# Kernel optimization log

Measured on AMD Instinct MI355X. Metric: run time of the kernel, lower is better.

## Reference

```python
import jax, jax.numpy as jnp
import numpy as np

N, D, M = 100000, 128, 2048


def setup_inputs() -> dict:
    key = jax.random.key(0)
    k1, k2, k3, k4 = jax.random.split(key, 4)
    X = jax.random.normal(k1, (N, D), dtype=jnp.float32)
    Y = jax.random.normal(k2, (N, 1), dtype=jnp.float32)
    centers = jax.random.normal(k3, (M, D), dtype=jnp.float32)
    # alpha is a buffer produced by an inner Falkon solve; use small random values
    alpha = jax.random.normal(k4, (M, 1), dtype=jnp.float32) * 0.01
    sigma = jnp.asarray(1.0, dtype=jnp.float32)     # Gaussian kernel lengthscale (nn.Parameter)
    penalty = jnp.asarray(5.0, dtype=jnp.float32)   # lambda = exp(-penalty)
    return {"X": X, "Y": Y, "centers": centers, "alpha": alpha,
            "sigma": sigma, "penalty": penalty}


def _rbf_mmv(A, B, v, sigma):
    # Gaussian (RBF) kernel mat-vec: exp(-||a-b||^2 / (2 sigma^2)) @ v
    # A:[n,d], B:[m,d], v:[m,1] -> [n,1]
    a2 = jnp.sum(A * A, axis=-1, keepdims=True)          # [n,1]
    b2 = jnp.sum(B * B, axis=-1, keepdims=True).T        # [1,m]
    sq = a2 + b2 - 2.0 * (A @ B.T)                       # [n,m] squared distances
    Kmat = jnp.exp(-sq / (2.0 * sigma * sigma))
    return Kmat @ v


def reference(X, Y, centers, alpha, sigma, penalty):
    # loss = mean((K_NM @ alpha - Y)^2) + exp(-penalty) * alpha^T K_MM alpha
    preds = _rbf_mmv(X, centers, alpha, sigma)                     # [N,1]
    loss = jnp.mean((preds - Y) ** 2)
    pen = jnp.exp(-penalty)
    reg = pen * (alpha.T @ _rbf_mmv(centers, centers, alpha, sigma))  # [1,1]
    total = loss + reg[0, 0]
    return total, preds
```

## Files before the change

### kernel.cpp

```cpp
#include <hip/hip_runtime.h>
#include <stdint.h>

typedef short short8 __attribute__((ext_vector_type(8)));
typedef float f32x4 __attribute__((ext_vector_type(4)));

#define TILE 128

__device__ __forceinline__ unsigned short f32_to_bf16(float f) {
    uint32_t u = __builtin_bit_cast(uint32_t, f);
    u += 0x7FFFu + ((u >> 16) & 1u);
    return (unsigned short)(u >> 16);
}
__device__ __forceinline__ float bf16_to_f32(unsigned short h) {
    return __builtin_bit_cast(float, (uint32_t)h << 16);
}

__global__ void prep_kernel(const float* __restrict__ C,
                            const float* __restrict__ alpha,
                            const float* __restrict__ sigma,
                            unsigned short* __restrict__ Bp,
                            float2* __restrict__ cw,
                            float* __restrict__ acc)
{
    const int t = threadIdx.x;
    const int g = blockIdx.x;
    const int r = t >> 4;
    const int c16 = t & 15;
    const int R = g * 16 + r;

    if (g == 0 && t == 0) {
        acc[0] = 0.f; acc[1] = 0.f;
        ((unsigned int*)acc)[2] = 0u;
    }

    const float4* src = (const float4*)(C + (size_t)R * 128 + c16 * 8);
    float4 va = src[0], vb = src[1];
    unsigned short h[8];
    h[0] = f32_to_bf16(va.x); h[1] = f32_to_bf16(va.y);
    h[2] = f32_to_bf16(va.z); h[3] = f32_to_bf16(va.w);
    h[4] = f32_to_bf16(vb.x); h[5] = f32_to_bf16(vb.y);
    h[6] = f32_to_bf16(vb.z); h[7] = f32_to_bf16(vb.w);
    float ss = 0.f;
    #pragma unroll
    for (int k = 0; k < 8; ++k) {
        float f = bf16_to_f32(h[k]);
        ss = fmaf(f, f, ss);
    }
    uint4 pk;
    pk.x = (uint32_t)h[0] | ((uint32_t)h[1] << 16);
    pk.y = (uint32_t)h[2] | ((uint32_t)h[3] << 16);
    pk.z = (uint32_t)h[4] | ((uint32_t)h[5] << 16);
    pk.w = (uint32_t)h[6] | ((uint32_t)h[7] << 16);
    *reinterpret_cast<uint4*>(Bp + (size_t)g * 2048 + c16 * 128 + r * 8) = pk;

    ss += __shfl_xor(ss, 1);
    ss += __shfl_xor(ss, 2);
    ss += __shfl_xor(ss, 4);
    ss += __shfl_xor(ss, 8);
    if (c16 == 0) {
        float sig = sigma[0];
        float q = 0.7213475204444817f / (sig * sig);
        cw[R] = make_float2(ss * q, alpha[R]);
    }
}

__global__ __launch_bounds__(512, 4)
void fused_kernel(const float* __restrict__ X, int N,
                  const float* __restrict__ Yv,
                  const unsigned short* __restrict__ Bp,
                  const float2* __restrict__ cw,
                  const float* __restrict__ alpha,
                  const float* __restrict__ sigma,
                  const float* __restrict__ penalty,
                  int nA, int nMt, int nBlk,
                  float* __restrict__ preds_out,
                  float* __restrict__ out0,
                  float* __restrict__ acc)
{
    __shared__ __align__(16) unsigned short ldsA[16384];
    __shared__ float a2p[TILE][4];
    __shared__ float predbuf[TILE][4];

    const int t    = threadIdx.x;
    const int lane = t & 63;
    const int wid  = t >> 6;
    const int h    = wid & 1;
    const int wq   = wid >> 1;
    const int l15  = lane & 15;
    const int quad = lane >> 4;

    const float sig = sigma[0];
    const float q  = 0.7213475204444817f / (sig * sig);
    const float q2 = 2.0f * q;

    const bool regmode = (int)blockIdx.x >= nA;
    int rowbase;
    float rowterm[4][4];
    short8 a[16];

    if (!regmode) {
        rowbase = blockIdx.x * TILE;
        const int r_  = t >> 2;
        const int qtr = t & 3;
        const int grow = rowbase + r_;
        unsigned short* dstbase = ldsA + (r_ >> 4) * 2048 + (r_ & 15) * 8;
        float ss = 0.f;
        if (grow < N) {
            const float4* src = (const float4*)(X + (size_t)grow * 128 + qtr * 32);
            #pragma unroll
            for (int c = 0; c < 4; ++c) {
                float4 va = src[2 * c], vb = src[2 * c + 1];
                unsigned short h0 = f32_to_bf16(va.x), h1 = f32_to_bf16(va.y);
                unsigned short h2 = f32_to_bf16(va.z), h3 = f32_to_bf16(va.w);
                unsigned short h4 = f32_to_bf16(vb.x), h5 = f32_to_bf16(vb.y);
                unsigned short h6 = f32_to_bf16(vb.z), h7 = f32_to_bf16(vb.w);
                float f0 = bf16_to_f32(h0), f1 = bf16_to_f32(h1);
                float f2 = bf16_to_f32(h2), f3 = bf16_to_f32(h3);
                float f4 = bf16_to_f32(h4), f5 = bf16_to_f32(h5);
                float f6 = bf16_to_f32(h6), f7 = bf16_to_f32(h7);
                ss = fmaf(f0, f0, ss); ss = fmaf(f1, f1, ss);
                ss = fmaf(f2, f2, ss); ss = fmaf(f3, f3, ss);
                ss = fmaf(f4, f4, ss); ss = fmaf(f5, f5, ss);
                ss = fmaf(f6, f6, ss); ss = fmaf(f7, f7, ss);
                uint4 pk;
                pk.x = (uint32_t)h0 | ((uint32_t)h1 << 16);
                pk.y = (uint32_t)h2 | ((uint32_t)h3 << 16);
                pk.z = (uint32_t)h4 | ((uint32_t)h5 << 16);
                pk.w = (uint32_t)h6 | ((uint32_t)h7 << 16);
                *reinterpret_cast<uint4*>(dstbase + (qtr * 4 + c) * 128) = pk;
            }
        } else {
            uint4 z; z.x = z.y = z.z = z.w = 0u;
            #pragma unroll
            for (int c = 0; c < 4; ++c)
                *reinterpret_cast<uint4*>(dstbase + (qtr * 4 + c) * 128) = z;
        }
        a2p[r_][qtr] = ss;
        __syncthreads();
        #pragma unroll
        for (int i = 0; i < 4; ++i)
            #pragma unroll
            for (int r = 0; r < 4; ++r) {
                int rl = h * 64 + i * 16 + quad * 4 + r;
                rowterm[i][r] = (a2p[rl][0] + a2p[rl][1] + a2p[rl][2] + a2p[rl][3]) * q;
            }
        const unsigned short* aLds = ldsA + (size_t)(h * 4) * 2048 + lane * 8;
        #pragma unroll
        for (int i = 0; i < 4; ++i)
            #pragma unroll
            for (int kk = 0; kk < 4; ++kk)
                a[i * 4 + kk] = *reinterpret_cast<const short8*>(aLds + (size_t)i * 2048 + kk * 512);
    } else {
        const int b2 = (int)blockIdx.x - nA;
        rowbase = b2 * TILE;
        const unsigned short* aG = Bp + (size_t)(b2 * 8 + h * 4) * 2048 + lane * 8;
        #pragma unroll
        for (int i = 0; i < 4; ++i)
            #pragma unroll
            for (int kk = 0; kk < 4; ++kk)
                a[i * 4 + kk] = *reinterpret_cast<const short8*>(aG + (size_t)i * 2048 + kk * 512);
        #pragma unroll
        for (int i = 0; i < 4; ++i)
            #pragma unroll
            for (int r = 0; r < 4; ++r)
                rowterm[i][r] = cw[rowbase + h * 64 + i * 16 + quad * 4 + r].x;
    }

    float srow[4][4] = {};
    const int nG = nMt * 8;
    const int nGper = nG >> 2;
    const int g0 = wq * nGper;

    for (int s = 0; s < nGper; ++s) {
        const int g = g0 + s;

        const unsigned short* bG = Bp + (size_t)g * 2048 + lane * 8;
        short8 b[4];
        #pragma unroll
        for (int kk = 0; kk < 4; ++kk)
            b[kk] = *reinterpret_cast<const short8*>(bG + kk * 512);
        float2 cj = cw[g * 16 + l15];

        f32x4 acc4[4];
        #pragma unroll
        for (int i = 0; i < 4; ++i) acc4[i] = (f32x4){0.f, 0.f, 0.f, 0.f};
        #pragma unroll
        for (int kk = 0; kk < 4; ++kk)
            #pragma unroll
            for (int i = 0; i < 4; ++i)
                acc4[i] = __builtin_amdgcn_mfma_f32_16x16x32_bf16(
                    a[i * 4 + kk], b[kk], acc4[i], 0, 0, 0);

        #pragma unroll
        for (int i = 0; i < 4; ++i) {
            #pragma unroll
            for (int r = 0; r < 4; ++r) {
                float u = fmaf(acc4[i][r], q2, -(rowterm[i][r] + cj.x));
                float e = __builtin_amdgcn_exp2f(u);
                srow[i][r] = fmaf(e, cj.y, srow[i][r]);
            }
        }
    }

    #pragma unroll
    for (int i = 0; i < 4; ++i) {
        #pragma unroll
        for (int r = 0; r < 4; ++r) {
            int rl = h * 64 + i * 16 + quad * 4 + r;
            float v = srow[i][r];
            v += __shfl_xor(v, 1);
            v += __shfl_xor(v, 2);
            v += __shfl_xor(v, 4);
            v += __shfl_xor(v, 8);
            if (l15 == 0)
                predbuf[rl][wq] = v;
        }
    }
    __syncthreads();

    float contrib = 0.f;
    if (t < TILE) {
        int grow = rowbase + t;
        if (!regmode) {
            if (grow < N) {
                float pred = (predbuf[t][0] + predbuf[t][1]) +
                             (predbuf[t][2] + predbuf[t][3]);
                preds_out[grow] = pred;
                float d = pred - Yv[grow];
                contrib = d * d;
            }
        } else {
            float pred = (predbuf[t][0] + predbuf[t][1]) +
                         (predbuf[t][2] + predbuf[t][3]);
            contrib = alpha[grow] * pred;
        }
    }
    contrib += __shfl_xor(contrib, 1);
    contrib += __shfl_xor(contrib, 2);
    contrib += __shfl_xor(contrib, 4);
    contrib += __shfl_xor(contrib, 8);
    contrib += __shfl_xor(contrib, 16);
    contrib += __shfl_xor(contrib, 32);
    if (lane == 0 && wid < 2) atomicAdd(regmode ? (acc + 1) : (acc + 0), contrib);

    __syncthreads();
    if (t == 0) {
        __threadfence();
        unsigned int old = atomicAdd((unsigned int*)(acc + 2), 1u);
        if (old == (unsigned int)(nBlk - 1)) {
            float lv = atomicAdd(acc + 0, 0.0f);
            float rv = atomicAdd(acc + 1, 0.0f);
            out0[0] = lv / (float)N + __expf(-penalty[0]) * rv;
        }
    }
}

extern "C" void kernel_launch(void* const* d_in, const int* in_sizes, int n_in,
                              void* d_out, int out_size, void* d_ws, size_t ws_size,
                              hipStream_t stream) {
    const float* X       = (const float*)d_in[0];
    const float* Y       = (const float*)d_in[1];
    const float* centers = (const float*)d_in[2];
    const float* alpha   = (const float*)d_in[3];
    const float* sigma   = (const float*)d_in[4];
    const float* penalty = (const float*)d_in[5];
    float* out = (float*)d_out;

    const int N = in_sizes[1];
    const int M = in_sizes[3];

    unsigned short* Bp = (unsigned short*)d_ws;
    float2* cw = (float2*)((char*)d_ws + (size_t)M * 256);
    float* acc = (float*)((char*)d_ws + (size_t)M * 264);

    prep_kernel<<<M / 16, 256, 0, stream>>>(centers, alpha, sigma, Bp, cw, acc);

    const int nA  = (N + TILE - 1) / TILE;
    const int nMt = M / TILE;
    const int nBlk = nA + nMt;
    fused_kernel<<<nBlk, 512, 0, stream>>>(X, N, Y, Bp, cw, alpha, sigma, penalty,
                                           nA, nMt, nBlk, out + 1, out, acc);
}
```

Measured before the change: 200.8 us.

## Halve row tile to 64 with 256-thread blocks and put reg blocks first

Shrinks each block from 128 rows and 512 threads to 64 rows and 256 threads. Each wave now holds two A row-tiles instead of four and covers half of the center groups instead of a quarter, and launch bounds allow six blocks per CU. The K_MM regularization blocks move to the start of the grid so they are scheduled early rather than trailing, and the B pointer arithmetic is hoisted out of the loop. The trade-off is that each B tile loaded from global or L2 feeds half as many MFMAs, so B traffic per unit of compute doubles, in exchange for more blocks and better load balance across CUs.

```diff
diff --git a/kernel.cpp b/kernel.cpp
--- a/kernel.cpp
+++ b/kernel.cpp
@@ -3,8 +3,6 @@
 
 typedef short short8 __attribute__((ext_vector_type(8)));
 typedef float f32x4 __attribute__((ext_vector_type(4)));
-
-#define TILE 128
 
 __device__ __forceinline__ unsigned short f32_to_bf16(float f) {
     uint32_t u = __builtin_bit_cast(uint32_t, f);
@@ -64,7 +62,7 @@
     }
 }
 
-__global__ __launch_bounds__(512, 4)
+__global__ __launch_bounds__(256, 6)
 void fused_kernel(const float* __restrict__ X, int N,
                   const float* __restrict__ Yv,
                   const unsigned short* __restrict__ Bp,
@@ -72,20 +70,20 @@
                   const float* __restrict__ alpha,
                   const float* __restrict__ sigma,
                   const float* __restrict__ penalty,
-                  int nA, int nMt, int nBlk,
+                  int nR, int nMt, int nBlk,
                   float* __restrict__ preds_out,
                   float* __restrict__ out0,
                   float* __restrict__ acc)
 {
-    __shared__ __align__(16) unsigned short ldsA[16384];
-    __shared__ float a2p[TILE][4];
-    __shared__ float predbuf[TILE][4];
+    __shared__ __align__(16) unsigned short ldsA[8192];
+    __shared__ float a2p[64][4];
+    __shared__ float predbuf[64][2];
 
     const int t    = threadIdx.x;
     const int lane = t & 63;
     const int wid  = t >> 6;
     const int h    = wid & 1;
-    const int wq   = wid >> 1;
+    const int c    = wid >> 1;
     const int l15  = lane & 15;
     const int quad = lane >> 4;
 
@@ -93,13 +91,13 @@
     const float q  = 0.7213475204444817f / (sig * sig);
     const float q2 = 2.0f * q;
 
-    const bool regmode = (int)blockIdx.x >= nA;
+    const bool regmode = (int)blockIdx.x < nR;
     int rowbase;
-    float rowterm[4][4];
-    short8 a[16];
+    float rowterm[2][4];
+    short8 a[8];
 
     if (!regmode) {
-        rowbase = blockIdx.x * TILE;
+        rowbase = ((int)blockIdx.x - nR) * 64;
         const int r_  = t >> 2;
         const int qtr = t & 3;
         const int grow = rowbase + r_;
@@ -108,8 +106,8 @@
         if (grow < N) {
             const float4* src = (const float4*)(X + (size_t)grow * 128 + qtr * 32);
             #pragma unroll
-            for (int c = 0; c < 4; ++c) {
-                float4 va = src[2 * c], vb = src[2 * c + 1];
+            for (int cc = 0; cc < 4; ++cc) {
+                float4 va = src[2 * cc], vb = src[2 * cc + 1];
                 unsigned short h0 = f32_to_bf16(va.x), h1 = f32_to_bf16(va.y);
                 unsigned short h2 = f32_to_bf16(va.z), h3 = f32_to_bf16(va.w);
                 unsigned short h4 = f32_to_bf16(vb.x), h5 = f32_to_bf16(vb.y);
@@ -127,72 +125,73 @@
                 pk.y = (uint32_t)h2 | ((uint32_t)h3 << 16);
                 pk.z = (uint32_t)h4 | ((uint32_t)h5 << 16);
                 pk.w = (uint32_t)h6 | ((uint32_t)h7 << 16);
-                *reinterpret_cast<uint4*>(dstbase + (qtr * 4 + c) * 128) = pk;
+                *reinterpret_cast<uint4*>(dstbase + (qtr * 4 + cc) * 128) = pk;
             }
         } else {
             uint4 z; z.x = z.y = z.z = z.w = 0u;
             #pragma unroll
-            for (int c = 0; c < 4; ++c)
-                *reinterpret_cast<uint4*>(dstbase + (qtr * 4 + c) * 128) = z;
+            for (int cc = 0; cc < 4; ++cc)
+                *reinterpret_cast<uint4*>(dstbase + (qtr * 4 + cc) * 128) = z;
         }
         a2p[r_][qtr] = ss;
         __syncthreads();
         #pragma unroll
-        for (int i = 0; i < 4; ++i)
+        for (int i = 0; i < 2; ++i)
             #pragma unroll
             for (int r = 0; r < 4; ++r) {
-                int rl = h * 64 + i * 16 + quad * 4 + r;
+                int rl = h * 32 + i * 16 + quad * 4 + r;
                 rowterm[i][r] = (a2p[rl][0] + a2p[rl][1] + a2p[rl][2] + a2p[rl][3]) * q;
             }
-        const unsigned short* aLds = ldsA + (size_t)(h * 4) * 2048 + lane * 8;
-        #pragma unroll
-        for (int i = 0; i < 4; ++i)
+        const unsigned short* aLds = ldsA + (size_t)(h * 2) * 2048 + lane * 8;
+        #pragma unroll
+        for (int i = 0; i < 2; ++i)
             #pragma unroll
             for (int kk = 0; kk < 4; ++kk)
                 a[i * 4 + kk] = *reinterpret_cast<const short8*>(aLds + (size_t)i * 2048 + kk * 512);
     } else {
-        const int b2 = (int)blockIdx.x - nA;
-        rowbase = b2 * TILE;
-        const unsigned short* aG = Bp + (size_t)(b2 * 8 + h * 4) * 2048 + lane * 8;
-        #pragma unroll
-        for (int i = 0; i < 4; ++i)
+        const int b2 = (int)blockIdx.x;
+        rowbase = b2 * 64;
+        const unsigned short* aG = Bp + (size_t)(b2 * 4 + h * 2) * 2048 + lane * 8;
+        #pragma unroll
+        for (int i = 0; i < 2; ++i)
             #pragma unroll
             for (int kk = 0; kk < 4; ++kk)
                 a[i * 4 + kk] = *reinterpret_cast<const short8*>(aG + (size_t)i * 2048 + kk * 512);
         #pragma unroll
-        for (int i = 0; i < 4; ++i)
+        for (int i = 0; i < 2; ++i)
             #pragma unroll
             for (int r = 0; r < 4; ++r)
-                rowterm[i][r] = cw[rowbase + h * 64 + i * 16 + quad * 4 + r].x;
-    }
-
-    float srow[4][4] = {};
+                rowterm[i][r] = cw[rowbase + h * 32 + i * 16 + quad * 4 + r].x;
+    }
+
+    float srow[2][4] = {};
     const int nG = nMt * 8;
-    const int nGper = nG >> 2;
-    const int g0 = wq * nGper;
+    const int nGper = nG >> 1;
+    const int g0 = c * nGper;
+
+    const unsigned short* bBase = Bp + (size_t)g0 * 2048 + lane * 8;
+    const float2* cwBase = cw + g0 * 16 + l15;
 
     for (int s = 0; s < nGper; ++s) {
-        const int g = g0 + s;
-
-        const unsigned short* bG = Bp + (size_t)g * 2048 + lane * 8;
+        const unsigned short* bG = bBase + (size_t)s * 2048;
         short8 b[4];
         #pragma unroll
         for (int kk = 0; kk < 4; ++kk)
             b[kk] = *reinterpret_cast<const short8*>(bG + kk * 512);
-        float2 cj = cw[g * 16 + l15];
-
-        f32x4 acc4[4];
-        #pragma unroll
-        for (int i = 0; i < 4; ++i) acc4[i] = (f32x4){0.f, 0.f, 0.f, 0.f};
+        float2 cj = cwBase[s * 16];
+
+        f32x4 acc4[2];
+        #pragma unroll
+        for (int i = 0; i < 2; ++i) acc4[i] = (f32x4){0.f, 0.f, 0.f, 0.f};
         #pragma unroll
         for (int kk = 0; kk < 4; ++kk)
             #pragma unroll
-            for (int i = 0; i < 4; ++i)
+            for (int i = 0; i < 2; ++i)
                 acc4[i] = __builtin_amdgcn_mfma_f32_16x16x32_bf16(
                     a[i * 4 + kk], b[kk], acc4[i], 0, 0, 0);
 
         #pragma unroll
-        for (int i = 0; i < 4; ++i) {
+        for (int i = 0; i < 2; ++i) {
             #pragma unroll
             for (int r = 0; r < 4; ++r) {
                 float u = fmaf(acc4[i][r], q2, -(rowterm[i][r] + cj.x));
@@ -203,35 +202,33 @@
     }
 
     #pragma unroll
-    for (int i = 0; i < 4; ++i) {
+    for (int i = 0; i < 2; ++i) {
         #pragma unroll
         for (int r = 0; r < 4; ++r) {
-            int rl = h * 64 + i * 16 + quad * 4 + r;
+            int rl = h * 32 + i * 16 + quad * 4 + r;
             float v = srow[i][r];
             v += __shfl_xor(v, 1);
             v += __shfl_xor(v, 2);
             v += __shfl_xor(v, 4);
             v += __shfl_xor(v, 8);
             if (l15 == 0)
-                predbuf[rl][wq] = v;
+                predbuf[rl][c] = v;
         }
     }
     __syncthreads();
 
     float contrib = 0.f;
-    if (t < TILE) {
+    if (t < 64) {
         int grow = rowbase + t;
         if (!regmode) {
             if (grow < N) {
-                float pred = (predbuf[t][0] + predbuf[t][1]) +
-                             (predbuf[t][2] + predbuf[t][3]);
+                float pred = predbuf[t][0] + predbuf[t][1];
                 preds_out[grow] = pred;
                 float d = pred - Yv[grow];
                 contrib = d * d;
             }
         } else {
-            float pred = (predbuf[t][0] + predbuf[t][1]) +
-                         (predbuf[t][2] + predbuf[t][3]);
+            float pred = predbuf[t][0] + predbuf[t][1];
             contrib = alpha[grow] * pred;
         }
     }
@@ -241,7 +238,7 @@
     contrib += __shfl_xor(contrib, 8);
     contrib += __shfl_xor(contrib, 16);
     contrib += __shfl_xor(contrib, 32);
-    if (lane == 0 && wid < 2) atomicAdd(regmode ? (acc + 1) : (acc + 0), contrib);
+    if (t == 0) atomicAdd(regmode ? (acc + 1) : (acc + 0), contrib);
 
     __syncthreads();
     if (t == 0) {
@@ -275,9 +272,10 @@
 
     prep_kernel<<<M / 16, 256, 0, stream>>>(centers, alpha, sigma, Bp, cw, acc);
 
-    const int nA  = (N + TILE - 1) / TILE;
-    const int nMt = M / TILE;
-    const int nBlk = nA + nMt;
-    fused_kernel<<<nBlk, 512, 0, stream>>>(X, N, Y, Bp, cw, alpha, sigma, penalty,
-                                           nA, nMt, nBlk, out + 1, out, acc);
-}
+    const int nR  = M / 64;
+    const int nA  = (N + 63) / 64;
+    const int nMt = M / 128;
+    const int nBlk = nR + nA;
+    fused_kernel<<<nBlk, 256, 0, stream>>>(X, N, Y, Bp, cw, alpha, sigma, penalty,
+                                           nR, nMt, nBlk, out + 1, out, acc);
+}
```

Measured after the change: 207.4 us. +3.3%, slower.
